# Optimization experiments

Hardware: AMD Instinct MI355X
Metric: run time of the kernel (lower is better)

The kernel has to match this reference:

```python
import jax, jax.numpy as jnp
import numpy as np

K_F = 3
NUM = K_F * K_F - 1          # 8 non-center neighbors
IDX_REF = NUM // 2           # 4 (center insertion index)
PROP_TIME = 18
AFFINITY_GAMMA = 0.5
B, H, W = 4, 480, 640


def _bilinear(img, y, x):
    """Bilinear sample img [H,W] at float coords y,x [K,H,W]; zero outside."""
    Hh, Ww = img.shape
    y0 = jnp.floor(y)
    x0 = jnp.floor(x)

    def gather(yy, xx):
        valid = (yy >= 0) & (yy < Hh) & (xx >= 0) & (xx < Ww)
        yi = jnp.clip(yy.astype(jnp.int32), 0, Hh - 1)
        xi = jnp.clip(xx.astype(jnp.int32), 0, Ww - 1)
        return jnp.where(valid, img[yi, xi], 0.0)

    wy = y - y0
    wx = x - x0
    return ((1 - wy) * (1 - wx) * gather(y0, x0)
            + (1 - wy) * wx * gather(y0, x0 + 1)
            + wy * (1 - wx) * gather(y0 + 1, x0)
            + wy * wx * gather(y0 + 1, x0 + 1))


def _deform_prop(feat, dy, dx, aff):
    """Modulated deformable 3x3 conv with all-ones weight, zero bias, ch=1.
    feat [B,1,H,W]; dy,dx,aff [B,9,H,W]. Output = sum_k aff_k * sample_k."""
    b, _, h, w = feat.shape
    ky = jnp.array([-1, -1, -1, 0, 0, 0, 1, 1, 1], feat.dtype)
    kx = jnp.array([-1, 0, 1, -1, 0, 1, -1, 0, 1], feat.dtype)
    gy = jnp.arange(h, dtype=feat.dtype)[:, None]   # [H,1]
    gx = jnp.arange(w, dtype=feat.dtype)[None, :]   # [1,W]
    py = gy[None, None] + ky[None, :, None, None] + dy  # [B,9,H,W]
    px = gx[None, None] + kx[None, :, None, None] + dx
    samp = jax.vmap(_bilinear)(feat[:, 0], py, px)      # [B,9,H,W]
    return jnp.sum(samp * aff, axis=1, keepdims=True)


def _affinity_normalization(aff, scale):
    # TGASS: tanh / (gamma*num), abs-sum normalize (clamped at 1), reference = 1 - sum
    aff = jnp.tanh(aff) / (scale + 1e-8)
    s = jnp.sum(jnp.abs(aff), axis=1, keepdims=True) + 1e-4
    s = jnp.maximum(s, 1.0)
    aff = aff / s
    aff_ref = 1.0 - jnp.sum(aff, axis=1, keepdims=True)
    return jnp.concatenate([aff[:, :IDX_REF], aff_ref, aff[:, IDX_REF:]], axis=1)


def setup_inputs() -> dict:
    key = jax.random.key(0)
    k1, k2, k3, k4, k5 = jax.random.split(key, 5)
    feat_init = jax.random.uniform(k1, (B, 1, H, W), jnp.float32) * 10.0
    guidance = jax.random.normal(k2, (B, 24, H, W), jnp.float32)
    confidence = jax.random.uniform(k3, (B, 1, H, W), jnp.float32)
    dense = jax.random.uniform(k4, (B, 1, H, W), jnp.float32) * 10.0
    mask = (jax.random.uniform(k5, (B, 1, H, W)) < 0.05).astype(jnp.float32)
    feat_fix = dense * mask
    aff_scale_const = jnp.full((1,), AFFINITY_GAMMA * NUM, jnp.float32)
    return {"feat_init": feat_init, "guidance": guidance,
            "confidence": confidence, "feat_fix": feat_fix,
            "aff_scale_const": aff_scale_const}


def reference(feat_init, guidance, confidence, feat_fix, aff_scale_const):
    b = feat_init.shape[0]
    h, w = feat_init.shape[2], feat_init.shape[3]
    # offsets: chunk guidance into (o1, o2, aff), interleave, insert zero at center
    o1, o2, aff_g = jnp.split(guidance, 3, axis=1)
    off = jnp.concatenate([o1, o2], axis=1).reshape(b, NUM, 2, h, w)
    zc = jnp.zeros((b, 1, 2, h, w), off.dtype)
    off = jnp.concatenate([off[:, :IDX_REF], zc, off[:, IDX_REF:]], axis=1)
    dy, dx = off[:, :, 0], off[:, :, 1]          # [B,9,H,W]
    aff = _affinity_normalization(aff_g, aff_scale_const)

    # preserve_input: fixed-pixel mask (ch_f == 1)
    mask_fix = (feat_fix > 0.0).astype(feat_init.dtype)
    conf = (1.0 - mask_fix) * confidence + mask_fix
    feat = (1.0 - mask_fix) * feat_init + mask_fix * feat_fix

    def step(f, _):
        f = _deform_prop(f * conf, dy, dx, aff)
        f = (1.0 - mask_fix) * f + mask_fix * feat_fix
        return f, None

    feat, _ = jax.lax.scan(step, feat, None, length=PROP_TIME)
    return feat
```

## Files before the change

kernel.cpp:

```cpp
#include <hip/hip_runtime.h>
#include <hip/hip_fp16.h>


#define HH 480
#define WW 640
#define BB 4
#define HWSZ (HH * WW)
#define NPIX (BB * HWSZ)
#define PROP_T 18
#define SLACK 704
#define NTHR 256
#define PXT 5
#define NBLK (NPIX / (NTHR * PXT))

struct f2u { float x, y; };

__device__ __forceinline__ float fast_tanh(float x) {
    x = fminf(fmaxf(x, -15.0f), 15.0f);
    float e = __expf(2.0f * x);
    return __fdividef(e - 1.0f, e + 1.0f);
}

__device__ __forceinline__ float affinities(const float* gb, float inv_scale,
                                            float t[8]) {
    float ssum = 1e-4f;
#pragma unroll
    for (int j = 0; j < 8; ++j) {
        float v = fast_tanh(gb[(16 + j) * HWSZ]) * inv_scale;
        t[j] = v; ssum += fabsf(v);
    }
    ssum = fmaxf(ssum, 1.0f);
    float rs = __fdividef(1.0f, ssum);
    float asum = 0.0f;
#pragma unroll
    for (int j = 0; j < 8; ++j) { t[j] *= rs; asum += t[j]; }
    return 1.0f - asum;
}

__device__ __forceinline__ void make_desc(int y, int x, int k,
                                          float dy, float dx, float ak,
                                          unsigned& pk, unsigned short& akh) {
    float py = (float)(y + k / 3 - 1) + dy;
    float px = (float)(x + k % 3 - 1) + dx;
    float y0f = floorf(py), x0f = floorf(px);
    float wy = py - y0f, wx = px - x0f;
    int y0 = (int)y0f, x0 = (int)x0f;
    if (y0 == -1)                 { ak *= wy;        wy = 1.0f; }
    else if (y0 == HH - 1)        { ak *= 1.0f - wy; wy = 0.0f; }
    else if (y0 < -1 || y0 >= HH) { ak = 0.0f; }
    if (x0 == -1)                 { ak *= wx;        wx = 1.0f; }
    else if (x0 == WW - 1)        { ak *= 1.0f - wx; wx = 0.0f; }
    else if (x0 < -1 || x0 >= WW) { ak = 0.0f; }
    int rel;
    if (ak == 0.0f) {
        rel = 0; wy = 0.0f; wx = 0.0f;
    } else {
        int yc = min(max(y0, -1), HH - 1);
        int xc = min(max(x0, -1), WW - 1);
        rel = (yc - y) * WW + (xc - x);
        rel = min(max(rel, -32767), 32767);
    }
    unsigned uy = (unsigned)(int)(wy * 255.0f + 0.5f);
    unsigned ux = (unsigned)(int)(wx * 255.0f + 0.5f);
    pk  = ((unsigned)(unsigned short)(short)rel << 16) | (uy << 8) | ux;
    akh = __half_as_ushort(__float2half(ak));
}

__device__ __forceinline__ float sample_rel(const float* __restrict__ fp,
                                            unsigned pk, unsigned short akh,
                                            float acc) {
    int rel = (int)(short)(pk >> 16);
    float wy = (float)((pk >> 8) & 0xffu) * (1.0f / 255.0f);
    float wx = (float)(pk & 0xffu) * (1.0f / 255.0f);
    float ak = __half2float(__ushort_as_half(akh));
    const float* p = fp + rel;
    f2u r0 = *reinterpret_cast<const f2u*>(p);
    f2u r1 = *reinterpret_cast<const f2u*>(p + WW);
    float bot = ak * wy;
    float top = ak - bot;
    float omwx = 1.0f - wx;
    acc = fmaf(top * omwx, r0.x, acc);
    acc = fmaf(top * wx,   r0.y, acc);
    acc = fmaf(bot * omwx, r1.x, acc);
    acc = fmaf(bot * wx,   r1.y, acc);
    return acc;
}

__global__ __launch_bounds__(NTHR) void precompute_kernel(
    const float* __restrict__ feat_init,
    const float* __restrict__ guid,
    const float* __restrict__ confidence,
    const float* __restrict__ feat_fix,
    const float* __restrict__ aff_scale,
    float* __restrict__ g0,
    unsigned* __restrict__ pk1Arr,
    unsigned short* __restrict__ akArr,
    uint2* __restrict__ cfArr) {
    const int pix = blockIdx.x * NTHR + threadIdx.x;
    const int b = pix / HWSZ;
    const int q = pix - b * HWSZ;
    const int y = q / WW;
    const int x = q - y * WW;
    const float* gb = guid + (size_t)b * 24 * HWSZ + q;

    float ff = feat_fix[pix];
    float m  = (ff > 0.0f) ? 1.0f : 0.0f;
    float km = 1.0f - m;
    float conf = km * confidence[pix] + m;
    float f0   = km * feat_init[pix] + m * ff;
    g0[pix] = f0 * conf;

    const float inv_scale = __fdividef(1.0f, aff_scale[0] + 1e-8f);
    float t[8];
    float aref = affinities(gb, inv_scale, t);
    uint2 cf;
    cf.x = ((unsigned)__half_as_ushort(__float2half(aref)) << 16)
         | (unsigned)__half_as_ushort(__float2half(conf));
    cf.y = __float_as_uint(m * ff);
    cfArr[pix] = cf;

    unsigned pk[8];
    unsigned short akh[8];
#pragma unroll
    for (int n = 0; n < 8; ++n) {
        const int k = (n < 4) ? n : (n + 1);
        float dy = gb[(2 * n) * HWSZ];
        float dx = gb[(2 * n + 1) * HWSZ];
        make_desc(y, x, k, dy, dx, t[n], pk[n], akh[n]);
    }
    uint4* pd = reinterpret_cast<uint4*>(pk1Arr) + 2 * pix;
    pd[0] = make_uint4(pk[0], pk[1], pk[2], pk[3]);
    pd[1] = make_uint4(pk[4], pk[5], pk[6], pk[7]);
    uint4 kv;
    kv.x = (unsigned)akh[0] | ((unsigned)akh[1] << 16);
    kv.y = (unsigned)akh[2] | ((unsigned)akh[3] << 16);
    kv.z = (unsigned)akh[4] | ((unsigned)akh[5] << 16);
    kv.w = (unsigned)akh[6] | ((unsigned)akh[7] << 16);
    reinterpret_cast<uint4*>(akArr)[pix] = kv;
}

__global__ __launch_bounds__(NTHR, 4) void persist_kernel(
    const unsigned* __restrict__ pk1Arr,
    const unsigned short* __restrict__ akArr,
    const uint2* __restrict__ cfArr,
    float* __restrict__ fA,
    float* __restrict__ fB,
    float* __restrict__ out,
    int* __restrict__ bar)
{
    __shared__ uint4 akS[NTHR * PXT];
    __shared__ uint2 cfS[NTHR * PXT];

    const int base = blockIdx.x * (NTHR * PXT) + threadIdx.x;

    uint4 pka[PXT], pkb[PXT];

#pragma unroll
    for (int i = 0; i < PXT; ++i) {
        const int pix = base + i * NTHR;
        const uint4* pd = reinterpret_cast<const uint4*>(pk1Arr) + 2 * pix;
        pka[i] = pd[0];
        pkb[i] = pd[1];
        akS[i * NTHR + threadIdx.x] = reinterpret_cast<const uint4*>(akArr)[pix];
        cfS[i * NTHR + threadIdx.x] = cfArr[pix];
    }
    __syncthreads();

#pragma unroll 1
    for (int t = 0; t < PROP_T; ++t) {
        const float* fin = (t & 1) ? fB : fA;
        float* fout = (t == PROP_T - 1) ? out : ((t & 1) ? fA : fB);
        const bool last = (t == PROP_T - 1);
#pragma unroll
        for (int i = 0; i < PXT; ++i) {
            const int pix = base + i * NTHR;
            const float* fp = fin + pix;
            uint4 K = akS[i * NTHR + threadIdx.x];
            uint2 c2 = cfS[i * NTHR + threadIdx.x];
            float aref = __half2float(__ushort_as_half((unsigned short)(c2.x >> 16)));
            float conf = __half2float(__ushort_as_half((unsigned short)(c2.x & 0xffffu)));
            float acc = aref * fp[0];
            uint4 A = pka[i], B = pkb[i];
            acc = sample_rel(fp, A.x, (unsigned short)(K.x & 0xffffu), acc);
            acc = sample_rel(fp, A.y, (unsigned short)(K.x >> 16),     acc);
            acc = sample_rel(fp, A.z, (unsigned short)(K.y & 0xffffu), acc);
            acc = sample_rel(fp, A.w, (unsigned short)(K.y >> 16),     acc);
            __builtin_amdgcn_sched_barrier(0);
            acc = sample_rel(fp, B.x, (unsigned short)(K.z & 0xffffu), acc);
            acc = sample_rel(fp, B.y, (unsigned short)(K.z >> 16),     acc);
            acc = sample_rel(fp, B.z, (unsigned short)(K.w & 0xffffu), acc);
            acc = sample_rel(fp, B.w, (unsigned short)(K.w >> 16),     acc);
            float mff = __uint_as_float(c2.y);
            float km = (mff > 0.0f) ? 0.0f : 1.0f;
            float fnew = fmaf(km, acc, mff);
            fout[pix] = last ? fnew : conf * fnew;
            __builtin_amdgcn_sched_barrier(0);
        }

        if (!last) {
            __syncthreads();
            if (threadIdx.x == 0) {
                __threadfence();
                atomicAdd(bar, 1);
                const int target = (t + 1) * NBLK;
                while (__hip_atomic_load(bar, __ATOMIC_ACQUIRE,
                                         __HIP_MEMORY_SCOPE_AGENT) < target) {
                    __builtin_amdgcn_s_sleep(4);
                }
                __threadfence();
            }
            __syncthreads();
        }
    }
}

__global__ __launch_bounds__(NTHR) void step_kernel(
    const float* __restrict__ fin,
    float* __restrict__ fout,
    const unsigned* __restrict__ pk1Arr,
    const unsigned short* __restrict__ akArr,
    const uint2* __restrict__ cfArr,
    int last) {
    const int pix = blockIdx.x * NTHR + threadIdx.x;
    const float* fp = fin + pix;
    const uint4* pd = reinterpret_cast<const uint4*>(pk1Arr) + 2 * pix;
    uint4 A = pd[0], B = pd[1];
    uint4 K = reinterpret_cast<const uint4*>(akArr)[pix];
    uint2 c2 = cfArr[pix];
    float aref = __half2float(__ushort_as_half((unsigned short)(c2.x >> 16)));
    float conf = __half2float(__ushort_as_half((unsigned short)(c2.x & 0xffffu)));
    float acc = aref * fp[0];
    acc = sample_rel(fp, A.x, (unsigned short)(K.x & 0xffffu), acc);
    acc = sample_rel(fp, A.y, (unsigned short)(K.x >> 16),     acc);
    acc = sample_rel(fp, A.z, (unsigned short)(K.y & 0xffffu), acc);
    acc = sample_rel(fp, A.w, (unsigned short)(K.y >> 16),     acc);
    acc = sample_rel(fp, B.x, (unsigned short)(K.z & 0xffffu), acc);
    acc = sample_rel(fp, B.y, (unsigned short)(K.z >> 16),     acc);
    acc = sample_rel(fp, B.z, (unsigned short)(K.w & 0xffffu), acc);
    acc = sample_rel(fp, B.w, (unsigned short)(K.w >> 16),     acc);
    float mff = __uint_as_float(c2.y);
    float km = (mff > 0.0f) ? 0.0f : 1.0f;
    float fnew = fmaf(km, acc, mff);
    fout[pix] = last ? fnew : conf * fnew;
}

extern "C" void kernel_launch(void* const* d_in, const int* in_sizes, int n_in,
                              void* d_out, int out_size, void* d_ws, size_t ws_size,
                              hipStream_t stream) {
    const float* feat_init  = (const float*)d_in[0];
    const float* guidance   = (const float*)d_in[1];
    const float* confidence = (const float*)d_in[2];
    const float* feat_fix   = (const float*)d_in[3];
    const float* aff_scale  = (const float*)d_in[4];

    const size_t bufFloats = (size_t)NPIX + 2 * SLACK;
    float* bufA = (float*)d_ws;
    float* bufB = bufA + bufFloats;
    unsigned* pk1Arr = (unsigned*)(bufB + bufFloats);
    unsigned short* akArr = (unsigned short*)(pk1Arr + 8 * (size_t)NPIX);
    uint2* cfArr = (uint2*)(akArr + 8 * (size_t)NPIX);
    int* barPtr = (int*)(cfArr + NPIX);
    float* fA = bufA + SLACK;
    float* fB = bufB + SLACK;
    float* outp = (float*)d_out;

    hipMemsetAsync(bufA, 0, SLACK * sizeof(float), stream);
    hipMemsetAsync(bufA + SLACK + NPIX, 0, SLACK * sizeof(float), stream);
    hipMemsetAsync(bufB, 0, SLACK * sizeof(float), stream);
    hipMemsetAsync(bufB + SLACK + NPIX, 0, SLACK * sizeof(float), stream);
    hipMemsetAsync(barPtr, 0, 128, stream);

    precompute_kernel<<<NPIX / NTHR, NTHR, 0, stream>>>(
        feat_init, guidance, confidence, feat_fix, aff_scale,
        fA, pk1Arr, akArr, cfArr);

    bool usePersist = false;
    {
        hipFuncAttributes fa{};
        if (hipFuncGetAttributes(&fa, reinterpret_cast<const void*>(persist_kernel))
                == hipSuccess && fa.localSizeBytes == 0) {
            int occ = 0;
            if (hipOccupancyMaxActiveBlocksPerMultiprocessor(
                    &occ, reinterpret_cast<const void*>(persist_kernel), NTHR,
                     0) == hipSuccess) {
                int dev = 0, cu = 0;
                hipGetDevice(&dev);
                hipDeviceGetAttribute(&cu, hipDeviceAttributeMultiprocessorCount, dev);
                if ((long)occ * cu >= NBLK) usePersist = true;
            }
        }
    }
    if (usePersist) {
        persist_kernel<<<NBLK, NTHR, 0, stream>>>(
            pk1Arr, akArr, cfArr, fA, fB, outp, barPtr);
        return;
    }

    for (int t = 0; t < PROP_T; ++t) {
        const float* fin = (t & 1) ? fB : fA;
        float* fout = (t == PROP_T - 1) ? outp : ((t & 1) ? fA : fB);
        step_kernel<<<NPIX / NTHR, NTHR, 0, stream>>>(
            fin, fout, pk1Arr, akArr, cfArr, (t == PROP_T - 1) ? 1 : 0);
    }
}
```

Measured before the change: 658.0 us.

## Replace persistent grid-barrier kernel with LDS-tiled per-step kernels and fallback gather

Drops the persistent kernel with its global atomic barrier and instead launches a 2D-tiled step kernel 18 times. Each block stages a 64x20 tile plus an 8-pixel halo of the feature map into shared memory and reads the bilinear taps from there. Taps that land outside the halo fall back to a precomputed global index array. This trades the grid-wide spin barrier and scattered global reads for per-step launch overhead, halo reload traffic and an extra index array.

```diff
diff --git a/kernel.cpp b/kernel.cpp
--- a/kernel.cpp
+++ b/kernel.cpp
@@ -10,10 +10,12 @@
 #define PROP_T 18
 #define SLACK 704
 #define NTHR 256
-#define PXT 5
-#define NBLK (NPIX / (NTHR * PXT))
-
-struct f2u { float x, y; };
+#define TW 64
+#define TH 20
+#define HALO 8
+#define TCW (TW + 2 * HALO)
+#define TR  (TH + 2 * HALO)
+#define SENT 0x7FFFu
 
 __device__ __forceinline__ float fast_tanh(float x) {
     x = fminf(fmaxf(x, -15.0f), 15.0f);
@@ -39,7 +41,9 @@
 
 __device__ __forceinline__ void make_desc(int y, int x, int k,
                                           float dy, float dx, float ak,
-                                          unsigned& pk, unsigned short& akh) {
+                                          int tY0, int tX0, int bBase,
+                                          unsigned& pkT, unsigned short& akh,
+                                          int& gidx) {
     float py = (float)(y + k / 3 - 1) + dy;
     float px = (float)(x + k % 3 - 1) + dx;
     float y0f = floorf(py), x0f = floorf(px);
@@ -51,38 +55,52 @@
     if (x0 == -1)                 { ak *= wx;        wx = 1.0f; }
     else if (x0 == WW - 1)        { ak *= 1.0f - wx; wx = 0.0f; }
     else if (x0 < -1 || x0 >= WW) { ak = 0.0f; }
-    int rel;
+
+    unsigned lrel;
     if (ak == 0.0f) {
-        rel = 0; wy = 0.0f; wx = 0.0f;
+        wy = 0.0f; wx = 0.0f;
+        lrel = (unsigned)((y - tY0 + HALO) * TCW + (x - tX0 + HALO));
+        gidx = bBase + y * WW + x;
     } else {
         int yc = min(max(y0, -1), HH - 1);
         int xc = min(max(x0, -1), WW - 1);
-        rel = (yc - y) * WW + (xc - x);
-        rel = min(max(rel, -32767), 32767);
+        gidx = bBase + yc * WW + xc;
+        int lyc = yc - tY0 + HALO;
+        int lxc = xc - tX0 + HALO;
+        lrel = (lyc >= 0 && lyc <= TR - 2 && lxc >= 0 && lxc <= TCW - 2)
+             ? (unsigned)(lyc * TCW + lxc) : SENT;
     }
     unsigned uy = (unsigned)(int)(wy * 255.0f + 0.5f);
     unsigned ux = (unsigned)(int)(wx * 255.0f + 0.5f);
-    pk  = ((unsigned)(unsigned short)(short)rel << 16) | (uy << 8) | ux;
+    pkT = (lrel << 16) | (uy << 8) | ux;
     akh = __half_as_ushort(__float2half(ak));
 }
 
-__device__ __forceinline__ float sample_rel(const float* __restrict__ fp,
-                                            unsigned pk, unsigned short akh,
-                                            float acc) {
-    int rel = (int)(short)(pk >> 16);
+__device__ __forceinline__ float samp(const float* __restrict__ tile,
+                                      const float* __restrict__ fin,
+                                      const int* __restrict__ gidxArr,
+                                      int pix, int n,
+                                      unsigned pk, unsigned short akh,
+                                      float acc) {
+    unsigned lrel = pk >> 16;
     float wy = (float)((pk >> 8) & 0xffu) * (1.0f / 255.0f);
     float wx = (float)(pk & 0xffu) * (1.0f / 255.0f);
     float ak = __half2float(__ushort_as_half(akh));
-    const float* p = fp + rel;
-    f2u r0 = *reinterpret_cast<const f2u*>(p);
-    f2u r1 = *reinterpret_cast<const f2u*>(p + WW);
+    float r00, r01, r10, r11;
+    if (__builtin_expect(lrel != SENT, 1)) {
+        const float* p = tile + lrel;
+        r00 = p[0]; r01 = p[1]; r10 = p[TCW]; r11 = p[TCW + 1];
+    } else {
+        const float* g = fin + gidxArr[(size_t)pix * 8 + n];
+        r00 = g[0]; r01 = g[1]; r10 = g[WW]; r11 = g[WW + 1];
+    }
     float bot = ak * wy;
     float top = ak - bot;
     float omwx = 1.0f - wx;
-    acc = fmaf(top * omwx, r0.x, acc);
-    acc = fmaf(top * wx,   r0.y, acc);
-    acc = fmaf(bot * omwx, r1.x, acc);
-    acc = fmaf(bot * wx,   r1.y, acc);
+    acc = fmaf(top * omwx, r00, acc);
+    acc = fmaf(top * wx,   r01, acc);
+    acc = fmaf(bot * omwx, r10, acc);
+    acc = fmaf(bot * wx,   r11, acc);
     return acc;
 }
 
@@ -93,14 +111,18 @@
     const float* __restrict__ feat_fix,
     const float* __restrict__ aff_scale,
     float* __restrict__ g0,
-    unsigned* __restrict__ pk1Arr,
+    unsigned* __restrict__ pkTArr,
     unsigned short* __restrict__ akArr,
-    uint2* __restrict__ cfArr) {
+    uint2* __restrict__ cfArr,
+    int* __restrict__ gidxArr) {
     const int pix = blockIdx.x * NTHR + threadIdx.x;
     const int b = pix / HWSZ;
     const int q = pix - b * HWSZ;
     const int y = q / WW;
     const int x = q - y * WW;
+    const int bBase = b * HWSZ;
+    const int tY0 = (y / TH) * TH;
+    const int tX0 = (x / TW) * TW;
     const float* gb = guid + (size_t)b * 24 * HWSZ + q;
 
     float ff = feat_fix[pix];
@@ -121,14 +143,15 @@
 
     unsigned pk[8];
     unsigned short akh[8];
+    int gi[8];
 #pragma unroll
     for (int n = 0; n < 8; ++n) {
         const int k = (n < 4) ? n : (n + 1);
         float dy = gb[(2 * n) * HWSZ];
         float dx = gb[(2 * n + 1) * HWSZ];
-        make_desc(y, x, k, dy, dx, t[n], pk[n], akh[n]);
-    }
-    uint4* pd = reinterpret_cast<uint4*>(pk1Arr) + 2 * pix;
+        make_desc(y, x, k, dy, dx, t[n], tY0, tX0, bBase, pk[n], akh[n], gi[n]);
+    }
+    uint4* pd = reinterpret_cast<uint4*>(pkTArr) + 2 * (size_t)pix;
     pd[0] = make_uint4(pk[0], pk[1], pk[2], pk[3]);
     pd[1] = make_uint4(pk[4], pk[5], pk[6], pk[7]);
     uint4 kv;
@@ -137,111 +160,64 @@
     kv.z = (unsigned)akh[4] | ((unsigned)akh[5] << 16);
     kv.w = (unsigned)akh[6] | ((unsigned)akh[7] << 16);
     reinterpret_cast<uint4*>(akArr)[pix] = kv;
-}
-
-__global__ __launch_bounds__(NTHR, 4) void persist_kernel(
-    const unsigned* __restrict__ pk1Arr,
+    int4* gd = reinterpret_cast<int4*>(gidxArr) + 2 * (size_t)pix;
+    gd[0] = make_int4(gi[0], gi[1], gi[2], gi[3]);
+    gd[1] = make_int4(gi[4], gi[5], gi[6], gi[7]);
+}
+
+__global__ __launch_bounds__(NTHR) void step_tile_kernel(
+    const float* __restrict__ fin,
+    float* __restrict__ fout,
+    const unsigned* __restrict__ pkTArr,
     const unsigned short* __restrict__ akArr,
     const uint2* __restrict__ cfArr,
-    float* __restrict__ fA,
-    float* __restrict__ fB,
-    float* __restrict__ out,
-    int* __restrict__ bar)
+    const int* __restrict__ gidxArr,
+    int last)
 {
-    __shared__ uint4 akS[NTHR * PXT];
-    __shared__ uint2 cfS[NTHR * PXT];
-
-    const int base = blockIdx.x * (NTHR * PXT) + threadIdx.x;
-
-    uint4 pka[PXT], pkb[PXT];
-
-#pragma unroll
-    for (int i = 0; i < PXT; ++i) {
-        const int pix = base + i * NTHR;
-        const uint4* pd = reinterpret_cast<const uint4*>(pk1Arr) + 2 * pix;
-        pka[i] = pd[0];
-        pkb[i] = pd[1];
-        akS[i * NTHR + threadIdx.x] = reinterpret_cast<const uint4*>(akArr)[pix];
-        cfS[i * NTHR + threadIdx.x] = cfArr[pix];
+    __shared__ float tile[TR * TCW];
+    const int tX0 = blockIdx.x * TW;
+    const int tY0 = blockIdx.y * TH;
+    const int b   = blockIdx.z;
+    const int bBase = b * HWSZ;
+    const int lx = threadIdx.x & 63;
+    const int ry = threadIdx.x >> 6;
+
+    const int y0g = tY0 - HALO;
+    const int x0g = tX0 - HALO;
+    for (int j = threadIdx.x; j < TR * TCW; j += NTHR) {
+        int r = j / TCW, c = j - r * TCW;
+        int gy = y0g + r, gx = x0g + c;
+        float v = 0.0f;
+        if (gy >= 0 && gy < HH && gx >= 0 && gx < WW)
+            v = fin[bBase + gy * WW + gx];
+        tile[j] = v;
     }
     __syncthreads();
 
-#pragma unroll 1
-    for (int t = 0; t < PROP_T; ++t) {
-        const float* fin = (t & 1) ? fB : fA;
-        float* fout = (t == PROP_T - 1) ? out : ((t & 1) ? fA : fB);
-        const bool last = (t == PROP_T - 1);
-#pragma unroll
-        for (int i = 0; i < PXT; ++i) {
-            const int pix = base + i * NTHR;
-            const float* fp = fin + pix;
-            uint4 K = akS[i * NTHR + threadIdx.x];
-            uint2 c2 = cfS[i * NTHR + threadIdx.x];
-            float aref = __half2float(__ushort_as_half((unsigned short)(c2.x >> 16)));
-            float conf = __half2float(__ushort_as_half((unsigned short)(c2.x & 0xffffu)));
-            float acc = aref * fp[0];
-            uint4 A = pka[i], B = pkb[i];
-            acc = sample_rel(fp, A.x, (unsigned short)(K.x & 0xffffu), acc);
-            acc = sample_rel(fp, A.y, (unsigned short)(K.x >> 16),     acc);
-            acc = sample_rel(fp, A.z, (unsigned short)(K.y & 0xffffu), acc);
-            acc = sample_rel(fp, A.w, (unsigned short)(K.y >> 16),     acc);
-            __builtin_amdgcn_sched_barrier(0);
-            acc = sample_rel(fp, B.x, (unsigned short)(K.z & 0xffffu), acc);
-            acc = sample_rel(fp, B.y, (unsigned short)(K.z >> 16),     acc);
-            acc = sample_rel(fp, B.z, (unsigned short)(K.w & 0xffffu), acc);
-            acc = sample_rel(fp, B.w, (unsigned short)(K.w >> 16),     acc);
-            float mff = __uint_as_float(c2.y);
-            float km = (mff > 0.0f) ? 0.0f : 1.0f;
-            float fnew = fmaf(km, acc, mff);
-            fout[pix] = last ? fnew : conf * fnew;
-            __builtin_amdgcn_sched_barrier(0);
-        }
-
-        if (!last) {
-            __syncthreads();
-            if (threadIdx.x == 0) {
-                __threadfence();
-                atomicAdd(bar, 1);
-                const int target = (t + 1) * NBLK;
-                while (__hip_atomic_load(bar, __ATOMIC_ACQUIRE,
-                                         __HIP_MEMORY_SCOPE_AGENT) < target) {
-                    __builtin_amdgcn_s_sleep(4);
-                }
-                __threadfence();
-            }
-            __syncthreads();
-        }
-    }
-}
-
-__global__ __launch_bounds__(NTHR) void step_kernel(
-    const float* __restrict__ fin,
-    float* __restrict__ fout,
-    const unsigned* __restrict__ pk1Arr,
-    const unsigned short* __restrict__ akArr,
-    const uint2* __restrict__ cfArr,
-    int last) {
-    const int pix = blockIdx.x * NTHR + threadIdx.x;
-    const float* fp = fin + pix;
-    const uint4* pd = reinterpret_cast<const uint4*>(pk1Arr) + 2 * pix;
-    uint4 A = pd[0], B = pd[1];
-    uint4 K = reinterpret_cast<const uint4*>(akArr)[pix];
-    uint2 c2 = cfArr[pix];
-    float aref = __half2float(__ushort_as_half((unsigned short)(c2.x >> 16)));
-    float conf = __half2float(__ushort_as_half((unsigned short)(c2.x & 0xffffu)));
-    float acc = aref * fp[0];
-    acc = sample_rel(fp, A.x, (unsigned short)(K.x & 0xffffu), acc);
-    acc = sample_rel(fp, A.y, (unsigned short)(K.x >> 16),     acc);
-    acc = sample_rel(fp, A.z, (unsigned short)(K.y & 0xffffu), acc);
-    acc = sample_rel(fp, A.w, (unsigned short)(K.y >> 16),     acc);
-    acc = sample_rel(fp, B.x, (unsigned short)(K.z & 0xffffu), acc);
-    acc = sample_rel(fp, B.y, (unsigned short)(K.z >> 16),     acc);
-    acc = sample_rel(fp, B.z, (unsigned short)(K.w & 0xffffu), acc);
-    acc = sample_rel(fp, B.w, (unsigned short)(K.w >> 16),     acc);
-    float mff = __uint_as_float(c2.y);
-    float km = (mff > 0.0f) ? 0.0f : 1.0f;
-    float fnew = fmaf(km, acc, mff);
-    fout[pix] = last ? fnew : conf * fnew;
+#pragma unroll
+    for (int i = 0; i < 5; ++i) {
+        const int yy = ry + 4 * i;
+        const int pix = bBase + (tY0 + yy) * WW + tX0 + lx;
+        const uint4* pd = reinterpret_cast<const uint4*>(pkTArr) + 2 * (size_t)pix;
+        uint4 A = pd[0], B = pd[1];
+        uint4 K = reinterpret_cast<const uint4*>(akArr)[pix];
+        uint2 c2 = cfArr[pix];
+        float aref = __half2float(__ushort_as_half((unsigned short)(c2.x >> 16)));
+        float conf = __half2float(__ushort_as_half((unsigned short)(c2.x & 0xffffu)));
+        float acc = aref * tile[(yy + HALO) * TCW + lx + HALO];
+        acc = samp(tile, fin, gidxArr, pix, 0, A.x, (unsigned short)(K.x & 0xffffu), acc);
+        acc = samp(tile, fin, gidxArr, pix, 1, A.y, (unsigned short)(K.x >> 16),     acc);
+        acc = samp(tile, fin, gidxArr, pix, 2, A.z, (unsigned short)(K.y & 0xffffu), acc);
+        acc = samp(tile, fin, gidxArr, pix, 3, A.w, (unsigned short)(K.y >> 16),     acc);
+        acc = samp(tile, fin, gidxArr, pix, 4, B.x, (unsigned short)(K.z & 0xffffu), acc);
+        acc = samp(tile, fin, gidxArr, pix, 5, B.y, (unsigned short)(K.z >> 16),     acc);
+        acc = samp(tile, fin, gidxArr, pix, 6, B.z, (unsigned short)(K.w & 0xffffu), acc);
+        acc = samp(tile, fin, gidxArr, pix, 7, B.w, (unsigned short)(K.w >> 16),     acc);
+        float mff = __uint_as_float(c2.y);
+        float km = (mff > 0.0f) ? 0.0f : 1.0f;
+        float fnew = fmaf(km, acc, mff);
+        fout[pix] = last ? fnew : conf * fnew;
+    }
 }
 
 extern "C" void kernel_launch(void* const* d_in, const int* in_sizes, int n_in,
@@ -256,10 +232,10 @@
     const size_t bufFloats = (size_t)NPIX + 2 * SLACK;
     float* bufA = (float*)d_ws;
     float* bufB = bufA + bufFloats;
-    unsigned* pk1Arr = (unsigned*)(bufB + bufFloats);
-    unsigned short* akArr = (unsigned short*)(pk1Arr + 8 * (size_t)NPIX);
+    unsigned* pkTArr = (unsigned*)(bufB + bufFloats);
+    unsigned short* akArr = (unsigned short*)(pkTArr + 8 * (size_t)NPIX);
     uint2* cfArr = (uint2*)(akArr + 8 * (size_t)NPIX);
-    int* barPtr = (int*)(cfArr + NPIX);
+    int* gidxArr = (int*)(cfArr + NPIX);
     float* fA = bufA + SLACK;
     float* fB = bufB + SLACK;
     float* outp = (float*)d_out;
@@ -268,38 +244,16 @@
     hipMemsetAsync(bufA + SLACK + NPIX, 0, SLACK * sizeof(float), stream);
     hipMemsetAsync(bufB, 0, SLACK * sizeof(float), stream);
     hipMemsetAsync(bufB + SLACK + NPIX, 0, SLACK * sizeof(float), stream);
-    hipMemsetAsync(barPtr, 0, 128, stream);
 
     precompute_kernel<<<NPIX / NTHR, NTHR, 0, stream>>>(
         feat_init, guidance, confidence, feat_fix, aff_scale,
-        fA, pk1Arr, akArr, cfArr);
-
-    bool usePersist = false;
-    {
-        hipFuncAttributes fa{};
-        if (hipFuncGetAttributes(&fa, reinterpret_cast<const void*>(persist_kernel))
-                == hipSuccess && fa.localSizeBytes == 0) {
-            int occ = 0;
-            if (hipOccupancyMaxActiveBlocksPerMultiprocessor(
-                    &occ, reinterpret_cast<const void*>(persist_kernel), NTHR,
-                     0) == hipSuccess) {
-                int dev = 0, cu = 0;
-                hipGetDevice(&dev);
-                hipDeviceGetAttribute(&cu, hipDeviceAttributeMultiprocessorCount, dev);
-                if ((long)occ * cu >= NBLK) usePersist = true;
-            }
-        }
-    }
-    if (usePersist) {
-        persist_kernel<<<NBLK, NTHR, 0, stream>>>(
-            pk1Arr, akArr, cfArr, fA, fB, outp, barPtr);
-        return;
-    }
-
+        fA, pkTArr, akArr, cfArr, gidxArr);
+
+    dim3 grd(WW / TW, HH / TH, BB);
     for (int t = 0; t < PROP_T; ++t) {
         const float* fin = (t & 1) ? fB : fA;
         float* fout = (t == PROP_T - 1) ? outp : ((t & 1) ? fA : fB);
-        step_kernel<<<NPIX / NTHR, NTHR, 0, stream>>>(
-            fin, fout, pk1Arr, akArr, cfArr, (t == PROP_T - 1) ? 1 : 0);
-    }
-}
+        step_tile_kernel<<<grd, NTHR, 0, stream>>>(
+            fin, fout, pkTArr, akArr, cfArr, gidxArr, (t == PROP_T - 1) ? 1 : 0);
+    }
+}
```

New measurement: 715.1 us. 8.7% more time.
